# Kernel tuning notes

Measured on AMD Instinct MI355X. Metric: run time of the kernel, lower is better.

The kernel has to match this reference:

```python
import jax, jax.numpy as jnp
import numpy as np

DT = 1.0          # config['IZHIK_TIME_STEP']
SURR_SCALE = 1.0  # ArcTan surrogate alpha
SURR_WIDTH = 20.0 # ArcTan surrogate width

@jax.custom_vjp
def spike_fn(x):
    # heaviside forward, ArcTan surrogate backward
    return (x > 0.0).astype(x.dtype)

def _spike_fwd(x):
    return spike_fn(x), x

def _spike_bwd(x, g):
    return (g * SURR_SCALE / (1.0 + (SURR_WIDTH * x) ** 2),)

spike_fn.defvjp(_spike_fwd, _spike_bwd)

B, T, N = 256, 500, 256

def setup_inputs() -> dict:
    key = jax.random.key(0)
    ks = jax.random.split(key, 14)
    input_batch = jax.random.normal(ks[0], (B, T, N), dtype=jnp.float32)
    state_snn = jnp.zeros((3, B, N), jnp.float32)   # (v, u, s)
    state_LI = jnp.zeros((B, 1), jnp.float32)
    W1 = jax.random.normal(ks[1], (N, N), jnp.float32) / np.sqrt(N)
    W2 = jax.random.normal(ks[2], (1, N), jnp.float32) / np.sqrt(N)
    def jit_param(k, base):
        return jnp.float32(base) * (1.0 + 0.1 * jax.random.uniform(k, (N,), jnp.float32))
    a      = jit_param(ks[3], 0.02)
    b      = jit_param(ks[4], 0.2)
    c      = jit_param(ks[5], -65.0)
    d      = jit_param(ks[6], 8.0)
    v0     = jit_param(ks[7], 140.0)
    v1     = jit_param(ks[8], 5.0)
    v2     = jit_param(ks[9], 0.04)
    tau_u  = jit_param(ks[10], 1.0)
    thresh = jit_param(ks[11], 30.0)
    leak   = jnp.full((1,), 0.9, jnp.float32)
    return dict(input_batch=input_batch, state_snn=state_snn, state_LI=state_LI,
                W1=W1, W2=W2, a=a, b=b, c=c, d=d, v0=v0, v1=v1, v2=v2,
                tau_u=tau_u, thresh=thresh, leak=leak)

def reference(input_batch, state_snn, state_LI, W1, W2, a, b, c, d, v0, v1, v2, tau_u, thresh, leak):
    x_seq = jnp.swapaxes(input_batch, 0, 1)  # [T, B, N]
    v_init, u_init, s_init = state_snn[0], state_snn[1], state_snn[2]

    def step(carry, x_t):
        v, u, s_prev, li = carry
        I = x_t @ W1.T                                        # [B, N] feedforward current
        v_mid = v + DT * (v2 * v * v + v1 * v + v0 - u + I)   # membrane update
        u_mid = u + (DT / tau_u) * a * (b * v - u)            # recovery update
        s = spike_fn(v_mid - thresh)                          # spike with surrogate grad
        v_new = v_mid * (1.0 - s) + s * c                     # reset v -> c on spike
        u_new = u_mid + s * d                                 # u += d on spike
        li_new = leak * li + (1.0 - leak) * (s @ W2.T)        # leaky-integrator readout [B,1]
        state_out = jnp.stack([v_new, u_new, s])              # [3, B, N]
        return (v_new, u_new, s, li_new), (s, state_out, li_new)

    _, (outputs, states_snn, decoded) = jax.lax.scan(
        step, (v_init, u_init, s_init, state_LI), x_seq)
    # outputs: [T, B, N]; states_snn: [T, 3, B, N]; decoded: [T, B, 1]
    return outputs, states_snn, decoded
```

## Files before the change

kernel.cpp:

```cpp
#include <hip/hip_runtime.h>

#define B_ 256
#define T_ 500
#define N_ 256
#define BN_ 65536
#define STP_ 196608
#define TW 64
#define NCHUNK 8

#define SOFT_BAR() do {                                   \
    __builtin_amdgcn_sched_barrier(0);                    \
    asm volatile("s_waitcnt lgkmcnt(0)" ::: "memory");    \
    __builtin_amdgcn_s_barrier();                         \
    __builtin_amdgcn_sched_barrier(0);                    \
} while (0)

__global__ __launch_bounds__(256)
void fused_snn_kernel(const float* __restrict__ X, const float* __restrict__ W1,
                      float* __restrict__ out_s, float* __restrict__ states,
                      float* __restrict__ out_dec,
                      const float* __restrict__ st_snn, const float* __restrict__ st_li,
                      const float* __restrict__ W2,
                      const float* __restrict__ pa, const float* __restrict__ pb,
                      const float* __restrict__ pc, const float* __restrict__ pd,
                      const float* __restrict__ pv0, const float* __restrict__ pv1,
                      const float* __restrict__ pv2, const float* __restrict__ ptau,
                      const float* __restrict__ pth, const float* __restrict__ pleak) {
    __shared__ float Xl[TW * 256];
    __shared__ float Il[TW * 256];
    __shared__ float Ws[2][8 * 256];
    __shared__ unsigned long long dotm[T_][4];

    const int bb   = blockIdx.x;
    const int tid  = threadIdx.x;
    const int w    = tid >> 6;
    const int lane = tid & 63;
    const int boff = bb * 256 + tid;

    float v = st_snn[boff];
    float u = st_snn[BN_ + boff];
    const float a_   = pa[tid];
    const float b_   = pb[tid];
    const float c_   = pc[tid];
    const float d_   = pd[tid];
    const float v0_  = pv0[tid];
    const float v1_  = pv1[tid];
    const float v2_  = pv2[tid];
    const float coef = (1.0f / ptau[tid]) * a_;
    const float th_  = pth[tid];

    const int g   = tid >> 5;
    const int tg  = g << 3;
    const int h4  = (tid & 31) << 2;

    const float* Xb = X + (size_t)bb * (T_ * 256);
    const int tl = tid & 63;
    const int wq = (tid >> 6) << 2;

    const float* Wr0 = W1 + (size_t)tid * 256;
    const float4 z0 = *(const float4*)(Wr0 + 0);
    const float4 z1 = *(const float4*)(Wr0 + 4);

    float4 ra[16];
    {
        const float* Xrow = Xb + (size_t)tl * 256;
#pragma unroll
        for (int r = 0; r < 16; ++r)
            ra[r] = *(const float4*)(Xrow + r * 16 + wq);
    }
#pragma unroll
    for (int r = 0; r < 16; ++r) {
        const int k = r * 16 + wq;
        Xl[(k + 0) * 64 + tl] = ra[r].x;
        Xl[(k + 1) * 64 + tl] = ra[r].y;
        Xl[(k + 2) * 64 + tl] = ra[r].z;
        Xl[(k + 3) * 64 + tl] = ra[r].w;
    }
    {
        float* Wd = &Ws[0][0];
        Wd[0*256+tid]=z0.x; Wd[1*256+tid]=z0.y; Wd[2*256+tid]=z0.z; Wd[3*256+tid]=z0.w;
        Wd[4*256+tid]=z1.x; Wd[5*256+tid]=z1.y; Wd[6*256+tid]=z1.z; Wd[7*256+tid]=z1.w;
    }
    SOFT_BAR();

    float Inx = 0.f;

    for (int cc = 0; cc < NCHUNK; ++cc) {
        const int tb = (cc - 1) * TW;

        float acc[8][8];
#pragma unroll
        for (int i = 0; i < 8; ++i)
#pragma unroll
            for (int j = 0; j < 8; ++j) acc[i][j] = 0.f;

        for (int ks = 0; ks < 32; ++ks) {
            float4 q0, q1;
            if (ks < 31) {
                const float* Wr = W1 + (size_t)tid * 256 + (ks + 1) * 8;
                q0 = *(const float4*)(Wr);
                q1 = *(const float4*)(Wr + 4);
            }
            if (ks == 24 && cc + 1 < NCHUNK) {
                const int t0n    = (cc + 1) * TW;
                const int validn = (T_ - t0n < TW) ? (T_ - t0n) : TW;
                const int tsrc   = t0n + ((tl < validn) ? tl : (validn - 1));
                const float* Xrow = Xb + (size_t)tsrc * 256;
#pragma unroll
                for (int r = 0; r < 16; ++r)
                    ra[r] = *(const float4*)(Xrow + r * 16 + wq);
            }
            const float* Wc = &Ws[ks & 1][0];
            const int kbase = ks << 3;
#pragma unroll
            for (int kk = 0; kk < 8; ++kk) {
                const float4 a0 = *(const float4*)&Xl[(kbase + kk) * 64 + tg];
                const float4 a1 = *(const float4*)&Xl[(kbase + kk) * 64 + tg + 4];
                const float4 b0 = *(const float4*)&Wc[kk * 256 + h4];
                const float4 b1 = *(const float4*)&Wc[kk * 256 + h4 + 128];
                const float avr[8] = {a0.x, a0.y, a0.z, a0.w, a1.x, a1.y, a1.z, a1.w};
                const float bvr[8] = {b0.x, b0.y, b0.z, b0.w, b1.x, b1.y, b1.z, b1.w};
#pragma unroll
                for (int i = 0; i < 8; ++i)
#pragma unroll
                    for (int j = 0; j < 8; ++j)
                        acc[i][j] += avr[i] * bvr[j];
            }
            if (cc > 0) {
#pragma unroll
                for (int e = 0; e < 2; ++e) {
                    const int q = (ks << 1) + e;
                    const float Icur = Inx;
                    if (q + 1 < TW) Inx = Il[(q + 1) * 256 + tid];
                    const int t = tb + q;
                    const size_t pbase = (size_t)t * STP_ + boff;

                    const float m1 = v2_ * v;
                    const float t2 = v1_ * v;
                    const float P  = __builtin_fmaf(m1, v, t2);
                    const float Q  = (P + v0_) - u;
                    const float vm = v + (Q + Icur);
                    const float tb2 = __builtin_fmaf(b_, v, -u);
                    const float um = __builtin_fmaf(coef, tb2, u);

                    const bool  sp = (vm - th_) > 0.f;
                    const float s  = sp ? 1.f : 0.f;
                    v = sp ? c_ : vm;
                    u = sp ? (um + d_) : um;

                    states[pbase]           = v;
                    states[pbase + BN_]     = u;
                    states[pbase + 2 * BN_] = s;
                    out_s[(size_t)t * BN_ + boff] = s;

                    const unsigned long long mset = __ballot(sp);
                    if (lane == 0) dotm[t][w] = mset;
                }
            }
            if (ks < 31) {
                float* Wd = &Ws[(ks + 1) & 1][0];
                Wd[0*256+tid]=q0.x; Wd[1*256+tid]=q0.y; Wd[2*256+tid]=q0.z; Wd[3*256+tid]=q0.w;
                Wd[4*256+tid]=q1.x; Wd[5*256+tid]=q1.y; Wd[6*256+tid]=q1.z; Wd[7*256+tid]=q1.w;
            }
            SOFT_BAR();
        }

#pragma unroll
        for (int i = 0; i < 8; ++i) {
            const int t = tg + i;
            *(float4*)&Il[t * 256 + h4] =
                make_float4(acc[i][0], acc[i][1], acc[i][2], acc[i][3]);
            *(float4*)&Il[t * 256 + h4 + 128] =
                make_float4(acc[i][4], acc[i][5], acc[i][6], acc[i][7]);
        }
        if (cc + 1 < NCHUNK) {
#pragma unroll
            for (int r = 0; r < 16; ++r) {
                const int k = r * 16 + wq;
                Xl[(k + 0) * 64 + tl] = ra[r].x;
                Xl[(k + 1) * 64 + tl] = ra[r].y;
                Xl[(k + 2) * 64 + tl] = ra[r].z;
                Xl[(k + 3) * 64 + tl] = ra[r].w;
            }
            float* Wd = &Ws[0][0];
            Wd[0*256+tid]=z0.x; Wd[1*256+tid]=z0.y; Wd[2*256+tid]=z0.z; Wd[3*256+tid]=z0.w;
            Wd[4*256+tid]=z1.x; Wd[5*256+tid]=z1.y; Wd[6*256+tid]=z1.z; Wd[7*256+tid]=z1.w;
        }
        SOFT_BAR();
        Inx = Il[tid];
    }

    {
        const int tbE = 7 * TW;
        for (int q = 0; q < 52; ++q) {
            const float Icur = Inx;
            if (q + 1 < 52) Inx = Il[(q + 1) * 256 + tid];
            const int t = tbE + q;
            const size_t pbase = (size_t)t * STP_ + boff;

            const float m1 = v2_ * v;
            const float t2 = v1_ * v;
            const float P  = __builtin_fmaf(m1, v, t2);
            const float Q  = (P + v0_) - u;
            const float vm = v + (Q + Icur);
            const float tb2 = __builtin_fmaf(b_, v, -u);
            const float um = __builtin_fmaf(coef, tb2, u);

            const bool  sp = (vm - th_) > 0.f;
            const float s  = sp ? 1.f : 0.f;
            v = sp ? c_ : vm;
            u = sp ? (um + d_) : um;

            states[pbase]           = v;
            states[pbase + BN_]     = u;
            states[pbase + 2 * BN_] = s;
            out_s[(size_t)t * BN_ + boff] = s;

            const unsigned long long mset = __ballot(sp);
            if (lane == 0) dotm[t][w] = mset;
        }
    }
    __syncthreads();

    float* scr  = &Ws[0][0];
    float* w2l  = scr;
    float* dotf = scr + 256;
    w2l[tid] = W2[tid];
    __syncthreads();
    for (int p = tid; p < T_ * 4; p += 256) {
        const int t  = p >> 2;
        const int ww = p & 3;
        unsigned long long m = dotm[t][ww];
        const float* wl = &w2l[ww << 6];
        float sum = 0.f;
        while (m) {
            const int i = __builtin_ctzll(m);
            sum += wl[i];
            m &= (m - 1);
        }
        dotf[t * 4 + ww] = sum;
    }
    __syncthreads();

    if (tid == 0) {
        const float lk_  = pleak[0];
        const float olk_ = 1.0f - lk_;
        float li = st_li[bb];
        for (int t = 0; t < T_; ++t) {
            const float dot = (dotf[t*4+0] + dotf[t*4+1]) + (dotf[t*4+2] + dotf[t*4+3]);
            li = lk_ * li + olk_ * dot;
            out_dec[(size_t)t * 256 + bb] = li;
        }
    }
}

extern "C" void kernel_launch(void* const* d_in, const int* in_sizes, int n_in,
                              void* d_out, int out_size, void* d_ws, size_t ws_size,
                              hipStream_t stream) {
    const float* input  = (const float*)d_in[0];
    const float* st_snn = (const float*)d_in[1];
    const float* st_li  = (const float*)d_in[2];
    const float* W1     = (const float*)d_in[3];
    const float* W2     = (const float*)d_in[4];
    const float* pa     = (const float*)d_in[5];
    const float* pb     = (const float*)d_in[6];
    const float* pc     = (const float*)d_in[7];
    const float* pd     = (const float*)d_in[8];
    const float* pv0    = (const float*)d_in[9];
    const float* pv1    = (const float*)d_in[10];
    const float* pv2    = (const float*)d_in[11];
    const float* ptau   = (const float*)d_in[12];
    const float* pth    = (const float*)d_in[13];
    const float* pleak  = (const float*)d_in[14];

    float* out        = (float*)d_out;
    float* out_s      = out;
    float* out_states = out + (size_t)T_ * BN_;
    float* out_dec    = out + (size_t)T_ * BN_ + (size_t)T_ * STP_;

    fused_snn_kernel<<<dim3(B_), dim3(256), 0, stream>>>(
        input, W1, out_s, out_states, out_dec, st_snn, st_li, W2,
        pa, pb, pc, pd, pv0, pv1, pv2, ptau, pth, pleak);
}
```

Baseline: 362.5 us.

## Double block size to 512 threads and split GEMM micro-tile across them

Measured after the change: 338.9 us. -6.5%, faster.

```diff
diff --git a/kernel.cpp b/kernel.cpp
--- a/kernel.cpp
+++ b/kernel.cpp
@@ -7,6 +7,7 @@
 #define STP_ 196608
 #define TW 64
 #define NCHUNK 8
+#define NTHR 512
 
 #define SOFT_BAR() do {                                   \
     __builtin_amdgcn_sched_barrier(0);                    \
@@ -15,7 +16,7 @@
     __builtin_amdgcn_sched_barrier(0);                    \
 } while (0)
 
-__global__ __launch_bounds__(256)
+__global__ __launch_bounds__(NTHR)
 void fused_snn_kernel(const float* __restrict__ X, const float* __restrict__ W1,
                       float* __restrict__ out_s, float* __restrict__ states,
                       float* __restrict__ out_dec,
@@ -35,42 +36,42 @@
     const int tid  = threadIdx.x;
     const int w    = tid >> 6;
     const int lane = tid & 63;
-    const int boff = bb * 256 + tid;
+    const int pn   = tid & 255;
+    const int boff = bb * 256 + pn;
 
     float v = st_snn[boff];
     float u = st_snn[BN_ + boff];
-    const float a_   = pa[tid];
-    const float b_   = pb[tid];
-    const float c_   = pc[tid];
-    const float d_   = pd[tid];
-    const float v0_  = pv0[tid];
-    const float v1_  = pv1[tid];
-    const float v2_  = pv2[tid];
-    const float coef = (1.0f / ptau[tid]) * a_;
-    const float th_  = pth[tid];
-
-    const int g   = tid >> 5;
-    const int tg  = g << 3;
+    const float b_   = pb[pn];
+    const float c_   = pc[pn];
+    const float d_   = pd[pn];
+    const float v0_  = pv0[pn];
+    const float v1_  = pv1[pn];
+    const float v2_  = pv2[pn];
+    const float coef = (1.0f / ptau[pn]) * pa[pn];
+    const float th_  = pth[pn];
+
+    const int tg4 = (tid >> 5) << 2;
     const int h4  = (tid & 31) << 2;
 
     const float* Xb = X + (size_t)bb * (T_ * 256);
     const int tl = tid & 63;
     const int wq = (tid >> 6) << 2;
 
-    const float* Wr0 = W1 + (size_t)tid * 256;
-    const float4 z0 = *(const float4*)(Wr0 + 0);
-    const float4 z1 = *(const float4*)(Wr0 + 4);
-
-    float4 ra[16];
+    const int wn = tid >> 1;
+    const int wk = (tid & 1) << 2;
+
+    const float4 z0 = *(const float4*)(W1 + (size_t)wn * 256 + wk);
+
+    float4 ra[8];
     {
         const float* Xrow = Xb + (size_t)tl * 256;
 #pragma unroll
-        for (int r = 0; r < 16; ++r)
-            ra[r] = *(const float4*)(Xrow + r * 16 + wq);
-    }
-#pragma unroll
-    for (int r = 0; r < 16; ++r) {
-        const int k = r * 16 + wq;
+        for (int r = 0; r < 8; ++r)
+            ra[r] = *(const float4*)(Xrow + wq + (r << 5));
+    }
+#pragma unroll
+    for (int r = 0; r < 8; ++r) {
+        const int k = wq + (r << 5);
         Xl[(k + 0) * 64 + tl] = ra[r].x;
         Xl[(k + 1) * 64 + tl] = ra[r].y;
         Xl[(k + 2) * 64 + tl] = ra[r].z;
@@ -78,8 +79,10 @@
     }
     {
         float* Wd = &Ws[0][0];
-        Wd[0*256+tid]=z0.x; Wd[1*256+tid]=z0.y; Wd[2*256+tid]=z0.z; Wd[3*256+tid]=z0.w;
-        Wd[4*256+tid]=z1.x; Wd[5*256+tid]=z1.y; Wd[6*256+tid]=z1.z; Wd[7*256+tid]=z1.w;
+        Wd[(wk + 0) * 256 + wn] = z0.x;
+        Wd[(wk + 1) * 256 + wn] = z0.y;
+        Wd[(wk + 2) * 256 + wn] = z0.z;
+        Wd[(wk + 3) * 256 + wn] = z0.w;
     }
     SOFT_BAR();
 
@@ -88,18 +91,16 @@
     for (int cc = 0; cc < NCHUNK; ++cc) {
         const int tb = (cc - 1) * TW;
 
-        float acc[8][8];
-#pragma unroll
-        for (int i = 0; i < 8; ++i)
+        float acc[4][8];
+#pragma unroll
+        for (int i = 0; i < 4; ++i)
 #pragma unroll
             for (int j = 0; j < 8; ++j) acc[i][j] = 0.f;
 
         for (int ks = 0; ks < 32; ++ks) {
-            float4 q0, q1;
+            float4 q0;
             if (ks < 31) {
-                const float* Wr = W1 + (size_t)tid * 256 + (ks + 1) * 8;
-                q0 = *(const float4*)(Wr);
-                q1 = *(const float4*)(Wr + 4);
+                q0 = *(const float4*)(W1 + (size_t)wn * 256 + (ks + 1) * 8 + wk);
             }
             if (ks == 24 && cc + 1 < NCHUNK) {
                 const int t0n    = (cc + 1) * TW;
@@ -107,31 +108,30 @@
                 const int tsrc   = t0n + ((tl < validn) ? tl : (validn - 1));
                 const float* Xrow = Xb + (size_t)tsrc * 256;
 #pragma unroll
-                for (int r = 0; r < 16; ++r)
-                    ra[r] = *(const float4*)(Xrow + r * 16 + wq);
+                for (int r = 0; r < 8; ++r)
+                    ra[r] = *(const float4*)(Xrow + wq + (r << 5));
             }
             const float* Wc = &Ws[ks & 1][0];
             const int kbase = ks << 3;
 #pragma unroll
             for (int kk = 0; kk < 8; ++kk) {
-                const float4 a0 = *(const float4*)&Xl[(kbase + kk) * 64 + tg];
-                const float4 a1 = *(const float4*)&Xl[(kbase + kk) * 64 + tg + 4];
+                const float4 a0 = *(const float4*)&Xl[(kbase + kk) * 64 + tg4];
                 const float4 b0 = *(const float4*)&Wc[kk * 256 + h4];
                 const float4 b1 = *(const float4*)&Wc[kk * 256 + h4 + 128];
-                const float avr[8] = {a0.x, a0.y, a0.z, a0.w, a1.x, a1.y, a1.z, a1.w};
+                const float avr[4] = {a0.x, a0.y, a0.z, a0.w};
                 const float bvr[8] = {b0.x, b0.y, b0.z, b0.w, b1.x, b1.y, b1.z, b1.w};
 #pragma unroll
-                for (int i = 0; i < 8; ++i)
+                for (int i = 0; i < 4; ++i)
 #pragma unroll
                     for (int j = 0; j < 8; ++j)
                         acc[i][j] += avr[i] * bvr[j];
             }
-            if (cc > 0) {
+            if (cc > 0 && tid < 256) {
 #pragma unroll
                 for (int e = 0; e < 2; ++e) {
                     const int q = (ks << 1) + e;
                     const float Icur = Inx;
-                    if (q + 1 < TW) Inx = Il[(q + 1) * 256 + tid];
+                    if (q + 1 < TW) Inx = Il[(q + 1) * 256 + pn];
                     const int t = tb + q;
                     const size_t pbase = (size_t)t * STP_ + boff;
 
@@ -159,15 +159,17 @@
             }
             if (ks < 31) {
                 float* Wd = &Ws[(ks + 1) & 1][0];
-                Wd[0*256+tid]=q0.x; Wd[1*256+tid]=q0.y; Wd[2*256+tid]=q0.z; Wd[3*256+tid]=q0.w;
-                Wd[4*256+tid]=q1.x; Wd[5*256+tid]=q1.y; Wd[6*256+tid]=q1.z; Wd[7*256+tid]=q1.w;
+                Wd[(wk + 0) * 256 + wn] = q0.x;
+                Wd[(wk + 1) * 256 + wn] = q0.y;
+                Wd[(wk + 2) * 256 + wn] = q0.z;
+                Wd[(wk + 3) * 256 + wn] = q0.w;
             }
             SOFT_BAR();
         }
 
 #pragma unroll
-        for (int i = 0; i < 8; ++i) {
-            const int t = tg + i;
+        for (int i = 0; i < 4; ++i) {
+            const int t = tg4 + i;
             *(float4*)&Il[t * 256 + h4] =
                 make_float4(acc[i][0], acc[i][1], acc[i][2], acc[i][3]);
             *(float4*)&Il[t * 256 + h4 + 128] =
@@ -175,26 +177,28 @@
         }
         if (cc + 1 < NCHUNK) {
 #pragma unroll
-            for (int r = 0; r < 16; ++r) {
-                const int k = r * 16 + wq;
+            for (int r = 0; r < 8; ++r) {
+                const int k = wq + (r << 5);
                 Xl[(k + 0) * 64 + tl] = ra[r].x;
                 Xl[(k + 1) * 64 + tl] = ra[r].y;
                 Xl[(k + 2) * 64 + tl] = ra[r].z;
                 Xl[(k + 3) * 64 + tl] = ra[r].w;
             }
             float* Wd = &Ws[0][0];
-            Wd[0*256+tid]=z0.x; Wd[1*256+tid]=z0.y; Wd[2*256+tid]=z0.z; Wd[3*256+tid]=z0.w;
-            Wd[4*256+tid]=z1.x; Wd[5*256+tid]=z1.y; Wd[6*256+tid]=z1.z; Wd[7*256+tid]=z1.w;
+            Wd[(wk + 0) * 256 + wn] = z0.x;
+            Wd[(wk + 1) * 256 + wn] = z0.y;
+            Wd[(wk + 2) * 256 + wn] = z0.z;
+            Wd[(wk + 3) * 256 + wn] = z0.w;
         }
         SOFT_BAR();
-        Inx = Il[tid];
-    }
-
-    {
+        Inx = Il[pn];
+    }
+
+    if (tid < 256) {
         const int tbE = 7 * TW;
         for (int q = 0; q < 52; ++q) {
             const float Icur = Inx;
-            if (q + 1 < 52) Inx = Il[(q + 1) * 256 + tid];
+            if (q + 1 < 52) Inx = Il[(q + 1) * 256 + pn];
             const int t = tbE + q;
             const size_t pbase = (size_t)t * STP_ + boff;
 
@@ -225,9 +229,9 @@
     float* scr  = &Ws[0][0];
     float* w2l  = scr;
     float* dotf = scr + 256;
-    w2l[tid] = W2[tid];
+    if (tid < 256) w2l[tid] = W2[tid];
     __syncthreads();
-    for (int p = tid; p < T_ * 4; p += 256) {
+    for (int p = tid; p < T_ * 4; p += NTHR) {
         const int t  = p >> 2;
         const int ww = p & 3;
         unsigned long long m = dotm[t][ww];
@@ -278,7 +282,7 @@
     float* out_states = out + (size_t)T_ * BN_;
     float* out_dec    = out + (size_t)T_ * BN_ + (size_t)T_ * STP_;
 
-    fused_snn_kernel<<<dim3(B_), dim3(256), 0, stream>>>(
+    fused_snn_kernel<<<dim3(B_), dim3(NTHR), 0, stream>>>(
         input, W1, out_s, out_states, out_dec, st_snn, st_li, W2,
         pa, pb, pc, pd, pv0, pv1, pv2, ptau, pth, pleak);
 }
```
